# Optimization experiments

Measured on AMD Instinct MI355X. Metric: run time of the kernel, lower is better.

## Reference

```python
import jax, jax.numpy as jnp
import numpy as np

T, B, Z, ADIM = 96, 128, 32, 16
LEVELS, FACTOR = 3, 2


def setup_inputs() -> dict:
    key = jax.random.key(0)
    k1, k2, k3, k4 = jax.random.split(key, 4)
    eye = jnp.eye(Z, dtype=jnp.float32)
    obs = jax.random.normal(k1, (T, B, ADIM), jnp.float32)
    # A, D initialized near identity (module inits self.A/self.D as eye per level)
    A = eye + 0.02 * jax.random.normal(k2, (B, T, LEVELS, Z, Z), jnp.float32)
    C = 0.05 * jax.random.normal(k3, (B, T, ADIM, Z), jnp.float32)
    D = eye + 0.02 * jax.random.normal(k4, (B, T, LEVELS - 1, Z, Z), jnp.float32)
    return {"obs": obs, "A": A, "C": C, "D": D}


def _forward(obs, A, C, D):
    Tn, Bn, a_dim = obs.shape
    z = A.shape[-1]
    I = jnp.eye(z, dtype=obs.dtype)
    Q = 0.08 * I                              # process noise (z x z)
    O = 0.08 * I                              # higher-level process noise
    R = 0.03 * jnp.eye(a_dim, dtype=obs.dtype)
    sigma0 = 20.0 * I
    mu0 = jnp.zeros((Bn, z, 1), dtype=obs.dtype)
    obs_c = obs[..., None]                    # [T,B,a,1]

    # ---- higher-level latent chains (levels=3 => level indices {0,1}) ----
    f2 = FACTOR ** (LEVELS - 1)               # factor_level for l = levels-2
    mu_j = mu0 + 0.01                         # [B,z,1]
    # level 1 (top coupling level): mean jumps every f2 steps via A[:,t,levels-1]
    A2 = jnp.moveaxis(A[:, :, LEVELS - 1], 1, 0)   # [T,B,z,z]
    nj = (Tn - 1) // f2
    jump_A = A2[f2 * jnp.arange(1, nj + 1)]        # [nj,B,z,z]

    def jstep(m, At):
        mn = At @ m
        return mn, mn

    _, ms = jax.lax.scan(jstep, mu_j, jump_A)
    chain = jnp.concatenate([mu_j[None], ms], axis=0)      # [nj+1,B,z,1]
    tidx = jnp.arange(Tn)
    mean1 = chain[tidx // f2]                              # [T,B,z,1]
    # variance of level 1: sigma0 until the first jump, then zeros (faithful to source)
    var1 = jnp.broadcast_to(
        jnp.where((tidx < f2)[:, None, None, None], sigma0[None, None], 0.0),
        (Tn, Bn, z, z)).astype(obs.dtype)
    # level 0: mean stays zero; variance gets O from t>=FACTOR onward (faithful)
    mean0 = jnp.zeros((Tn, Bn, z, 1), dtype=obs.dtype)
    var0 = jnp.broadcast_to(
        jnp.where((tidx >= FACTOR)[:, None, None, None], O[None, None], 0.0),
        (Tn, Bn, z, z)).astype(obs.dtype)
    latent_means = jnp.stack([mean0, mean1], axis=2)       # [T,B,levels-1,z,1]
    latent_variances = jnp.stack([var0, var1], axis=2)     # [T,B,levels-1,z,z]

    # ---- main Kalman filter recursion over T ----
    C_t = jnp.moveaxis(C, 1, 0)                            # [T,B,a,z]
    A0 = jnp.moveaxis(A[:, :, 0], 1, 0)                    # [T,B,z,z]
    D0 = jnp.moveaxis(D[:, :, 0], 1, 0)                    # [T,B,z,z]
    pad_I = jnp.broadcast_to(I, (1, Bn, z, z))
    A_next = jnp.concatenate([A0[1:], pad_I], axis=0)      # A[:,t+1,0]; last unused
    D_next = jnp.concatenate([D0[1:], jnp.zeros_like(pad_I)], axis=0)

    def step(carry, xs):
        mu_t, sigma_t = carry
        o, Ct, An, Dn, m1, v1 = xs
        CT = jnp.swapaxes(Ct, -1, -2)
        r = o - Ct @ mu_t                                  # innovation [B,a,1]
        S = Ct @ sigma_t @ CT + R                          # [B,a,a]
        K = sigma_t @ CT @ jnp.linalg.inv(S)               # Kalman gain [B,z,a]
        mu_z = mu_t + K @ r
        I_ = I - K @ Ct
        sigma_z = I_ @ sigma_t @ jnp.swapaxes(I_, -1, -2) + K @ R @ jnp.swapaxes(K, -1, -2)
        mu_n = An @ mu_z + Dn @ m1
        sigma_n = An @ sigma_z @ jnp.swapaxes(An, -1, -2) + Q + Dn @ v1 @ jnp.swapaxes(Dn, -1, -2)
        return (mu_n, sigma_n), (mu_t, sigma_t, mu_z, sigma_z, S)

    init = (mu0, jnp.broadcast_to(sigma0, (Bn, z, z)).astype(obs.dtype))
    _, (mu_pred, sigma_pred, mu_filt, sigma_filt, S_tensor) = jax.lax.scan(
        step, init, (obs_c, C_t, A_next, D_next, mean1, var1))
    return (mu_filt, sigma_filt, mu_pred, sigma_pred,
            latent_means, latent_variances, S_tensor)


def reference(obs, A, C, D):
    return _forward(obs, A, C, D)
```

## Files before the change

### kernel.cpp

```cpp
#include <hip/hip_runtime.h>

typedef unsigned int uint;
typedef unsigned short ushort;

#define TT 96
#define BB 128

#define OFF_MUF   0
#define OFF_SIGF  393216
#define OFF_MUP   12976128
#define OFF_SIGP  13369344
#define OFF_LM    25952256
#define OFF_LV    26738688
#define OFF_ST    51904512

__device__ __forceinline__ float bf2f(uint u) {
  union { uint i; float f; } c; c.i = u << 16; return c.f;
}
__device__ __forceinline__ float bflo(uint w) { return bf2f(w & 0xffffu); }
__device__ __forceinline__ float bfhi(uint w) { return bf2f(w >> 16); }

__device__ __forceinline__ ushort f2bf(float f) {
  union { float f; uint i; } c; c.f = f;
  return (ushort)((c.i + 0x7fffu + ((c.i >> 16) & 1u)) >> 16);
}
__device__ __forceinline__ uint pack2(float a, float b) {
  return (uint)f2bf(a) | ((uint)f2bf(b) << 16);
}

__device__ __forceinline__ void split3(float x, ushort& h, ushort& m, ushort& l) {
  h = f2bf(x); float r = x - bf2f((uint)h);
  m = f2bf(r); r -= bf2f((uint)m);
  l = f2bf(r);
}

__device__ __forceinline__ float readlane_f(float x, int l) {
  return __int_as_float(__builtin_amdgcn_readlane(__float_as_int(x), l));
}

template<int F32>
__device__ __forceinline__ float4 ld4(const void* p, long e) {
  if constexpr (F32) {
    return *(const float4*)((const float*)p + e);
  } else {
    uint2 w = *(const uint2*)((const ushort*)p + e);
    return make_float4(bflo(w.x), bfhi(w.x), bflo(w.y), bfhi(w.y));
  }
}
template<int F32>
__device__ __forceinline__ float ld1(const void* p, long e) {
  if constexpr (F32) return ((const float*)p)[e];
  else               return bf2f((uint)((const ushort*)p)[e]);
}
template<int F32>
__device__ __forceinline__ void st4(void* p, long e, float4 v) {
  if constexpr (F32) {
    *(float4*)((float*)p + e) = v;
  } else {
    uint2 w; w.x = pack2(v.x, v.y); w.y = pack2(v.z, v.w);
    *(uint2*)((ushort*)p + e) = w;
  }
}
template<int F32>
__device__ __forceinline__ void st1(void* p, long e, float v) {
  if constexpr (F32) ((float*)p)[e] = v;
  else               ((ushort*)p)[e] = f2bf(v);
}

__device__ __forceinline__ bool data_is_f32(const void* A) {
  ushort h = ((const ushort*)A)[1];
  return (h & 0x7FFF) >= 0x3E80;
}

#define BAR() do { \
  __builtin_amdgcn_sched_barrier(0); \
  asm volatile("s_waitcnt lgkmcnt(0)" ::: "memory"); \
  __builtin_amdgcn_s_barrier(); \
  asm volatile("" ::: "memory"); \
  __builtin_amdgcn_sched_barrier(0); \
} while (0)

template<int F32>
__global__ void __launch_bounds__(256)
hkv_kernel(const void* __restrict__ obs, const void* __restrict__ A,
           const void* __restrict__ C, const void* __restrict__ D,
           void* __restrict__ out)
{
  if (data_is_f32(A) != (F32 == 1)) return;
  const int tid = threadIdx.x;

  if (blockIdx.x >= BB) {
    const int fb = blockIdx.x - BB;
    const int NG = (TT * BB * 2 * 32 * 32) / 4;
    for (int g = fb * 256 + tid; g < NG; g += BB * 256) {
      int e0 = g << 2;
      int R  = e0 >> 5;
      int c0 = e0 & 31;
      int zi = R & 31;
      int l  = (R >> 5) & 1;
      int t  = R >> 13;
      float dv = 0.0f;
      if (l == 0) { if (t >= 2) dv = 0.08f; }
      else        { if (t < 4)  dv = 20.0f; }
      float4 w = make_float4(0.f, 0.f, 0.f, 0.f);
      if (dv != 0.0f && zi >= c0 && zi < c0 + 4) ((float*)&w)[zi - c0] = dv;
      st4<F32>(out, OFF_LV + (long)e0, w);
    }
    return;
  }

  const int b    = blockIdx.x;
  const int lane = tid & 63;
  const int wv   = tid >> 6;

  __shared__ __align__(16) float sig[32][36];
  __shared__ __align__(16) float an[32][36];
  __shared__ __align__(16) float ant[32][36];
  __shared__ __align__(16) float dnm[32][36];
  __shared__ __align__(16) float asig[32][36];
  __shared__ __align__(16) float asAt[32][36];
  __shared__ __align__(16) float ct[16][36];
  __shared__ __align__(16) float cts[16][36];
  __shared__ __align__(16) float Vm[16][36];
  __shared__ __align__(16) float Ks[32][20];
  __shared__ __align__(16) float Um[32][20];
  __shared__ __align__(16) float Ss[16][20];
  __shared__ __align__(16) float ch[24][32];
  __shared__ float muv[32], muz[32], rv[16], yv[16], ov[16];

  for (int idx = tid; idx < 1024; idx += 256) {
    int i = idx >> 5, j = idx & 31;
    sig[i][j] = (i == j) ? 20.0f : 0.0f;
  }
  if (tid < 32) muv[tid] = 0.0f;

  if (tid < 32) {
    const int zi = tid;
    float m = 0.01f;
    ch[0][zi] = m;
    float cur[32], nxt[32];
    {
      long base = (((long)b * TT + 4) * 3 + 2) * 1024 + zi * 32;
      #pragma unroll
      for (int u = 0; u < 8; ++u) {
        float4 v = ld4<F32>(A, base + u * 4);
        nxt[4*u] = v.x; nxt[4*u+1] = v.y; nxt[4*u+2] = v.z; nxt[4*u+3] = v.w;
      }
    }
    for (int j = 1; j < 24; ++j) {
      #pragma unroll
      for (int u = 0; u < 32; ++u) cur[u] = nxt[u];
      if (j < 23) {
        long base = (((long)b * TT + 4 * (j + 1)) * 3 + 2) * 1024 + zi * 32;
        #pragma unroll
        for (int u = 0; u < 8; ++u) {
          float4 v = ld4<F32>(A, base + u * 4);
          nxt[4*u] = v.x; nxt[4*u+1] = v.y; nxt[4*u+2] = v.z; nxt[4*u+3] = v.w;
        }
      }
      float mp = m;
      float s = 0.0f;
      #pragma unroll
      for (int k = 0; k < 32; ++k) s = fmaf(cur[k], __shfl(mp, k, 64), s);
      m = s;
      ch[j][zi] = m;
    }
  }
  __syncthreads();

  for (int t = 0; t < TT; ++t) {
    const long tb = (long)t * BB + b;

    {
      int e0 = tid << 2;
      int i = e0 >> 5, j0 = e0 & 31;
      st4<F32>(out, OFF_SIGP + tb * 1024 + e0,
               make_float4(sig[i][j0], sig[i][j0+1], sig[i][j0+2], sig[i][j0+3]));
    }
    if (t < TT - 1) {
      int e0 = tid << 2; int i = e0 >> 5, j = e0 & 31;
      float4 a4 = ld4<F32>(A, ((long)(b * TT + t + 1) * 3) * 1024 + e0);
      an[i][j] = a4.x; an[i][j+1] = a4.y; an[i][j+2] = a4.z; an[i][j+3] = a4.w;
      ant[j][i] = a4.x; ant[j+1][i] = a4.y; ant[j+2][i] = a4.z; ant[j+3][i] = a4.w;
      float4 d4 = ld4<F32>(D, ((long)(b * TT + t + 1) * 2) * 1024 + e0);
      dnm[i][j] = d4.x; dnm[i][j+1] = d4.y; dnm[i][j+2] = d4.z; dnm[i][j+3] = d4.w;
    } else {
      int e0 = tid << 2; int i = e0 >> 5, j = e0 & 31;
      #pragma unroll
      for (int u = 0; u < 4; ++u) {
        float v = (i == j + u) ? 1.0f : 0.0f;
        an[i][j + u] = v; ant[j + u][i] = v; dnm[i][j + u] = 0.0f;
      }
    }
    if (tid < 128) {
      int e0 = tid << 2; int i = e0 >> 5, j = e0 & 31;
      float4 c4 = ld4<F32>(C, ((long)b * TT + t) * 512 + e0);
      ct[i][j] = c4.x; ct[i][j+1] = c4.y; ct[i][j+2] = c4.z; ct[i][j+3] = c4.w;
    } else if (tid < 192) {
      int l = (tid - 128) >> 5, zi = tid & 31;
      st1<F32>(out, OFF_LM + (tb * 2 + l) * 32 + zi, l ? ch[t >> 2][zi] : 0.0f);
    } else if (tid < 224) {
      int i = tid - 192;
      st1<F32>(out, OFF_MUP + tb * 32 + i, muv[i]);
    } else if (tid < 240) {
      int i = tid - 224;
      ov[i] = ld1<F32>(obs, tb * 16 + i);
    }
    __syncthreads();

    if (tid < 128) {
      int i = tid >> 3, j0 = (tid & 7) << 2;
      float4 acc = make_float4(0.f, 0.f, 0.f, 0.f);
      for (int k = 0; k < 32; ++k) {
        float a = ct[i][k];
        float4 s4 = *(const float4*)&sig[k][j0];
        acc.x = fmaf(a, s4.x, acc.x); acc.y = fmaf(a, s4.y, acc.y);
        acc.z = fmaf(a, s4.z, acc.z); acc.w = fmaf(a, s4.w, acc.w);
      }
      *(float4*)&cts[i][j0] = acc;
    } else if (tid < 144) {
      int i = tid - 128;
      float s = ov[i];
      for (int k = 0; k < 32; ++k) s = fmaf(-ct[i][k], muv[k], s);
      rv[i] = s;
    }
    __syncthreads();

    {
      int i = tid >> 4, j = tid & 15;
      float s = (i == j) ? 0.03f : 0.0f;
      for (int k = 0; k < 32; k += 4) {
        float4 a4 = *(const float4*)&cts[i][k];
        float4 b4 = *(const float4*)&ct[j][k];
        s += a4.x * b4.x + a4.y * b4.y + a4.z * b4.z + a4.w * b4.w;
      }
      Ss[i][j] = s;
      st1<F32>(out, OFF_ST + tb * 256 + tid, s);
    }
    __syncthreads();

    if (wv == 0) {
      const int r = lane >> 2, q = lane & 3;
      float v[13];
      #pragma unroll
      for (int m = 0; m < 13; ++m) {
        int c = 4 * m + q;
        float x = 0.0f;
        if (c < 16) x = Ss[r][c];
        else if (c < 48) x = cts[r][c - 16];
        else if (c == 48) x = rv[r];
        v[m] = x;
      }
      #pragma unroll
      for (int p = 0; p < 16; ++p) {
        const int mp = p >> 2, qp = p & 3;
        float pv = __shfl(v[mp], 4 * p + qp, 64);
        float f  = __shfl(v[mp], 4 * r + qp, 64);
        float rc = 1.0f / pv;
        #pragma unroll
        for (int m = 0; m < 13; ++m) {
          float srow = __shfl(v[m], 4 * p + q, 64) * rc;
          v[m] = (r == p) ? srow : fmaf(-f, srow, v[m]);
        }
      }
      #pragma unroll
      for (int m = 0; m < 13; ++m) {
        int c = 4 * m + q;
        if (c >= 16 && c < 48) Ks[c - 16][r] = v[m];
        else if (c == 48) yv[r] = v[m];
      }
    } else {
      int tt = tid - 64;
      for (int idx = tt; idx < 256; idx += 192) {
        int i = idx >> 3, j0 = (idx & 7) << 2;
        float4 acc = make_float4(0.f, 0.f, 0.f, 0.f);
        for (int k = 0; k < 32; ++k) {
          float a = an[i][k];
          float4 s4 = *(const float4*)&sig[k][j0];
          acc.x = fmaf(a, s4.x, acc.x); acc.y = fmaf(a, s4.y, acc.y);
          acc.z = fmaf(a, s4.z, acc.z); acc.w = fmaf(a, s4.w, acc.w);
        }
        *(float4*)&asig[i][j0] = acc;
      }
      for (int idx = tt; idx < 512; idx += 192) {
        int i = idx >> 5, j = idx & 31;
        float s = 0.0f;
        for (int k = 0; k < 32; k += 4) {
          float4 c4 = *(const float4*)&cts[i][k];
          float4 a4 = *(const float4*)&an[j][k];
          s += c4.x * a4.x + c4.y * a4.y + c4.z * a4.z + c4.w * a4.w;
        }
        Vm[i][j] = s;
      }
    }
    __syncthreads();

    {
      int i = tid >> 3, j0 = (tid & 7) << 2;
      float4 acc = make_float4(0.f, 0.f, 0.f, 0.f);
      for (int k = 0; k < 32; ++k) {
        float a = asig[i][k];
        float4 s4 = *(const float4*)&ant[k][j0];
        acc.x = fmaf(a, s4.x, acc.x); acc.y = fmaf(a, s4.y, acc.y);
        acc.z = fmaf(a, s4.z, acc.z); acc.w = fmaf(a, s4.w, acc.w);
      }
      int dd = i - j0;
      if (dd == 0) acc.x += 0.08f; else if (dd == 1) acc.y += 0.08f;
      else if (dd == 2) acc.z += 0.08f; else if (dd == 3) acc.w += 0.08f;
      *(float4*)&asAt[i][j0] = acc;

      float4 sz = *(const float4*)&sig[i][j0];
      for (int k = 0; k < 16; ++k) {
        float a = Ks[i][k];
        float4 c4 = *(const float4*)&cts[k][j0];
        sz.x = fmaf(-a, c4.x, sz.x); sz.y = fmaf(-a, c4.y, sz.y);
        sz.z = fmaf(-a, c4.z, sz.z); sz.w = fmaf(-a, c4.w, sz.w);
      }
      st4<F32>(out, OFF_SIGF + tb * 1024 + (i * 32 + j0), sz);
    }
    if (tid < 128) {
      int i = tid >> 2, j0 = (tid & 3) << 2;
      float4 acc = make_float4(0.f, 0.f, 0.f, 0.f);
      for (int k = 0; k < 32; ++k) {
        float a = an[i][k];
        float4 k4 = *(const float4*)&Ks[k][j0];
        acc.x = fmaf(a, k4.x, acc.x); acc.y = fmaf(a, k4.y, acc.y);
        acc.z = fmaf(a, k4.z, acc.z); acc.w = fmaf(a, k4.w, acc.w);
      }
      *(float4*)&Um[i][j0] = acc;
    } else if (tid < 160) {
      int i = tid - 128;
      float s = muv[i];
      for (int k = 0; k < 16; ++k) s = fmaf(cts[k][i], yv[k], s);
      muz[i] = s;
      st1<F32>(out, OFF_MUF + tb * 32 + i, s);
    }
    __syncthreads();

    {
      int i = tid >> 3, j0 = (tid & 7) << 2;
      float4 acc = *(const float4*)&asAt[i][j0];
      for (int k = 0; k < 16; ++k) {
        float u = Um[i][k];
        float4 v4 = *(const float4*)&Vm[k][j0];
        acc.x = fmaf(-u, v4.x, acc.x); acc.y = fmaf(-u, v4.y, acc.y);
        acc.z = fmaf(-u, v4.z, acc.z); acc.w = fmaf(-u, v4.w, acc.w);
      }
      if (t < 4) {
        float4 da = make_float4(0.f, 0.f, 0.f, 0.f);
        for (int k = 0; k < 32; ++k) {
          float a = dnm[i][k];
          da.x = fmaf(a, dnm[j0][k],     da.x);
          da.y = fmaf(a, dnm[j0 + 1][k], da.y);
          da.z = fmaf(a, dnm[j0 + 2][k], da.z);
          da.w = fmaf(a, dnm[j0 + 3][k], da.w);
        }
        acc.x += 20.0f * da.x; acc.y += 20.0f * da.y;
        acc.z += 20.0f * da.z; acc.w += 20.0f * da.w;
      }
      *(float4*)&sig[i][j0] = acc;
    }
    if (tid < 32) {
      int i = tid;
      float s = 0.0f;
      for (int k = 0; k < 32; ++k) s = fmaf(an[i][k], muz[k], s);
      const float* chr = ch[t >> 2];
      for (int k = 0; k < 32; ++k) s = fmaf(dnm[i][k], chr[k], s);
      muv[i] = s;
    }
    __syncthreads();
  }
}

typedef __attribute__((ext_vector_type(8))) short bf16x8;
typedef __attribute__((ext_vector_type(4))) float f32x4;

#define MFMA16(a, b, c) __builtin_amdgcn_mfma_f32_16x16x32_bf16((a), (b), (c), 0, 0, 0)

__global__ void __launch_bounds__(256)
hkv_f32(const void* __restrict__ obs, const void* __restrict__ A,
        const void* __restrict__ C, const void* __restrict__ D,
        void* __restrict__ out)
{
  if (!data_is_f32(A)) return;
  const int tid = threadIdx.x;
  float* outf = (float*)out;

  if (blockIdx.x >= BB) {
    const int fb = blockIdx.x - BB;
    const int NG = (TT * BB * 2 * 32 * 32) / 4;
    for (int g = fb * 256 + tid; g < NG; g += BB * 256) {
      int e0 = g << 2;
      int R  = e0 >> 5;
      int c0 = e0 & 31;
      int zi = R & 31;
      int l  = (R >> 5) & 1;
      int t  = R >> 13;
      float dv = 0.0f;
      if (l == 0) { if (t >= 2) dv = 0.08f; }
      else        { if (t < 4)  dv = 20.0f; }
      float4 w = make_float4(0.f, 0.f, 0.f, 0.f);
      if (dv != 0.0f && zi >= c0 && zi < c0 + 4) ((float*)&w)[zi - c0] = dv;
      st4<1>(out, OFF_LV + (long)e0, w);
    }
    return;
  }

  const int b    = blockIdx.x;
  const int lane = tid & 63;
  const int wv   = tid >> 6;
  const int tm   = wv >> 1;
  const int tn   = wv & 1;
  const int lr   = lane & 15;
  const int lk   = lane >> 4;
  const int lk8  = lk << 3;
  const int pi   = tid >> 3;
  const int pj   = (tid & 7) << 2;

  const float* Of = (const float*)obs;

  __shared__ __align__(16) ushort sg[3][32][40];
  __shared__ __align__(16) ushort an[3][32][40];
  __shared__ __align__(16) ushort dn[3][32][40];
  __shared__ __align__(16) ushort as_[3][32][40];
  __shared__ __align__(16) ushort ct[3][16][40];
  __shared__ __align__(16) ushort wt[3][16][40];
  __shared__ __align__(16) ushort kt[3][16][40];
  __shared__ __align__(16) ushort w_[3][32][24];
  __shared__ __align__(16) ushort ks[3][32][24];
  __shared__ __align__(16) ushort u_[3][32][24];
  __shared__ __align__(16) ushort aw[3][32][24];
  __shared__ __align__(16) float Ssf[16][20];
  __shared__ __align__(16) float wtf[16][36];
  __shared__ __align__(16) float ch[24][32];
  __shared__ __align__(16) float muv[32];
  __shared__ __align__(16) float muzv[32];
  __shared__ __align__(16) float rv[16];
  __shared__ __align__(16) float yv[16];
  __shared__ __align__(16) float ov[16];

  const bf16x8 z8 = {0, 0, 0, 0, 0, 0, 0, 0};
  #define F40(arr, rb) (*(const bf16x8*)&(arr)[(rb) + lr][lk8])
  #define F24(arr, rb) ((lk < 2) ? (*(const bf16x8*)&(arr)[(rb) + lr][lk8]) : z8)
  #define PROD_F(acc, X, xb, Y, yb) do { \
    bf16x8 xh_=F40(X[0],(xb)), xm_=F40(X[1],(xb)), xl_=F40(X[2],(xb)); \
    bf16x8 yh_=F40(Y[0],(yb)), ym_=F40(Y[1],(yb)), yl_=F40(Y[2],(yb)); \
    f32x4 a1_ = {0.f,0.f,0.f,0.f}; \
    acc=MFMA16(xh_,yh_,acc); a1_=MFMA16(xm_,yh_,a1_); \
    acc=MFMA16(xh_,ym_,acc); a1_=MFMA16(xl_,yh_,a1_); \
    acc=MFMA16(xh_,yl_,acc); a1_=MFMA16(xm_,ym_,a1_); \
    acc += a1_; } while(0)
  #define PROD_H(acc, X, xb, Y, yb) do { \
    bf16x8 xh_=F24(X[0],(xb)), xm_=F24(X[1],(xb)), xl_=F24(X[2],(xb)); \
    bf16x8 yh_=F24(Y[0],(yb)), ym_=F24(Y[1],(yb)), yl_=F24(Y[2],(yb)); \
    f32x4 a1_ = {0.f,0.f,0.f,0.f}; \
    acc=MFMA16(xh_,yh_,acc); a1_=MFMA16(xm_,yh_,a1_); \
    acc=MFMA16(xh_,ym_,acc); a1_=MFMA16(xl_,yh_,a1_); \
    acc=MFMA16(xh_,yl_,acc); a1_=MFMA16(xm_,ym_,a1_); \
    acc += a1_; } while(0)
  #define SPLW(ARR, rr, cc, x) do { ushort h_,m_,l_; split3((x),h_,m_,l_); \
    ARR[0][rr][cc]=h_; ARR[1][rr][cc]=m_; ARR[2][rr][cc]=l_; } while(0)

  float anc[4], dnc[4];
  {
    float4 a4 = ld4<1>(A, ((long)(b * TT + 1) * 3) * 1024 + (tid << 2));
    float4 d4 = ld4<1>(D, ((long)(b * TT + 1) * 2) * 1024 + (tid << 2));
    anc[0]=a4.x; anc[1]=a4.y; anc[2]=a4.z; anc[3]=a4.w;
    dnc[0]=d4.x; dnc[1]=d4.y; dnc[2]=d4.z; dnc[3]=d4.w;
    #pragma unroll
    for (int u = 0; u < 4; ++u) { SPLW(an, pi, pj+u, anc[u]); SPLW(dn, pi, pj+u, dnc[u]); }
  }
  if (tid < 128) {
    float4 c4 = ld4<1>(C, ((long)b * TT) * 512 + (tid << 2));
    float cc4[4] = {c4.x, c4.y, c4.z, c4.w};
    #pragma unroll
    for (int u = 0; u < 4; ++u) SPLW(ct, tid >> 3, ((tid & 7) << 2) + u, cc4[u]);
  } else if (tid < 144) {
    ov[tid - 128] = Of[(long)b * 16 + (tid - 128)];
  }
  for (int idx = tid; idx < 1024; idx += 256) {
    int i = idx >> 5, j = idx & 31;
    sg[0][i][j] = (i == j) ? 0x41A0 : 0;
    sg[1][i][j] = 0; sg[2][i][j] = 0;
  }
  if (tid < 32) muv[tid] = 0.0f;

  float sig_reg[4];
  #pragma unroll
  for (int v = 0; v < 4; ++v) {
    int rr = 16 * tm + lk * 4 + v, cc = 16 * tn + lr;
    sig_reg[v] = (rr == cc) ? 20.0f : 0.0f;
  }

  if (tid < 32) {
    const int zi = tid;
    float m = 0.01f;
    ch[0][zi] = m;
    float curv[32], nxtv[32];
    {
      long base = (((long)b * TT + 4) * 3 + 2) * 1024 + zi * 32;
      #pragma unroll
      for (int u = 0; u < 8; ++u) {
        float4 v = ld4<1>(A, base + u * 4);
        nxtv[4*u]=v.x; nxtv[4*u+1]=v.y; nxtv[4*u+2]=v.z; nxtv[4*u+3]=v.w;
      }
    }
    for (int j = 1; j < 24; ++j) {
      #pragma unroll
      for (int u = 0; u < 32; ++u) curv[u] = nxtv[u];
      if (j < 23) {
        long base = (((long)b * TT + 4 * (j + 1)) * 3 + 2) * 1024 + zi * 32;
        #pragma unroll
        for (int u = 0; u < 8; ++u) {
          float4 v = ld4<1>(A, base + u * 4);
          nxtv[4*u]=v.x; nxtv[4*u+1]=v.y; nxtv[4*u+2]=v.z; nxtv[4*u+3]=v.w;
        }
      }
      float mp = m, s = 0.0f;
      #pragma unroll
      for (int k = 0; k < 32; ++k) s = fmaf(curv[k], __shfl(mp, k, 64), s);
      m = s;
      ch[j][zi] = m;
    }
  }
  BAR();

  for (int t = 0; t < TT; ++t) {
    const long tb = (long)t * BB + b;

    {
      f32x4 acc = {0.f, 0.f, 0.f, 0.f};
      PROD_F(acc, an, 16 * tm, sg, 16 * tn);
      #pragma unroll
      for (int v = 0; v < 4; ++v) {
        int rr = 16 * tm + lk * 4 + v, cc = 16 * tn + lr;
        outf[OFF_SIGP + tb * 1024 + rr * 32 + cc] = sig_reg[v];
        SPLW(as_, rr, cc, acc[v]);
      }
    }
    if (wv >= 2) {
      const int a = wv - 2;
      f32x4 acc = {0.f, 0.f, 0.f, 0.f};
      PROD_F(acc, sg, 16 * a, ct, 0);
      #pragma unroll
      for (int v = 0; v < 4; ++v) {
        int row = 16 * a + lk * 4 + v;
        ushort h_, m_, l_; split3(acc[v], h_, m_, l_);
        w_[0][row][lr]=h_; w_[1][row][lr]=m_; w_[2][row][lr]=l_;
        wt[0][lr][row]=h_; wt[1][lr][row]=m_; wt[2][lr][row]=l_;
        wtf[lr][row] = acc[v];
      }
    } else if (wv == 0) {
      int i = lane & 15, kg = lane >> 4;
      float s = 0.0f;
      #pragma unroll
      for (int u = 0; u < 8; ++u) {
        int k = kg * 8 + u;
        float cv = bf2f((uint)ct[0][i][k]) + bf2f((uint)ct[1][i][k])
                 + bf2f((uint)ct[2][i][k]);
        s = fmaf(cv, muv[k], s);
      }
      s += __shfl_xor(s, 16, 64);
      s += __shfl_xor(s, 32, 64);
      if (kg == 0) rv[i] = ov[i] - s;
    } else {
      int l = lane >> 5, zi = lane & 31;
      outf[OFF_LM + (tb * 2 + l) * 32 + zi] = l ? ch[t >> 2][zi] : 0.0f;
      if (lane < 32) outf[OFF_MUP + tb * 32 + zi] = muv[zi];
    }
    BAR();

    float pa[4], pd[4], pc[4] = {0.f,0.f,0.f,0.f}; float pobs = 0.f;
    if (t < TT - 1) {
      if (t < TT - 2) {
        float4 a4 = ld4<1>(A, ((long)(b * TT + t + 2) * 3) * 1024 + (tid << 2));
        float4 d4 = ld4<1>(D, ((long)(b * TT + t + 2) * 2) * 1024 + (tid << 2));
        pa[0]=a4.x; pa[1]=a4.y; pa[2]=a4.z; pa[3]=a4.w;
        pd[0]=d4.x; pd[1]=d4.y; pd[2]=d4.z; pd[3]=d4.w;
      } else {
        #pragma unroll
        for (int u = 0; u < 4; ++u) { pa[u] = (pi == pj + u) ? 1.0f : 0.0f; pd[u] = 0.0f; }
      }
      if (tid < 128) {
        float4 c4 = ld4<1>(C, ((long)b * TT + (t + 1)) * 512 + (tid << 2));
        pc[0]=c4.x; pc[1]=c4.y; pc[2]=c4.z; pc[3]=c4.w;
      } else if (tid < 144) {
        pobs = Of[((long)(t + 1) * BB + b) * 16 + (tid - 128)];
      }
    }

    f32x4 acc_at = {0.f, 0.f, 0.f, 0.f};
    PROD_F(acc_at, as_, 16 * tm, an, 16 * tn);
    f32x4 acc_d = {0.f, 0.f, 0.f, 0.f};
    if (t < 4) PROD_F(acc_d, dn, 16 * tm, dn, 16 * tn);

    if (wv == 0) {
      f32x4 s4 = {0.f, 0.f, 0.f, 0.f};
      PROD_F(s4, wt, 0, ct, 0);
      #pragma unroll
      for (int v = 0; v < 4; ++v) {
        int r = lk * 4 + v;
        float val = s4[v] + ((r == lr) ? 0.03f : 0.0f);
        Ssf[r][lr] = val;
        outf[OFF_ST + tb * 256 + r * 16 + lr] = val;
      }
      const int c = lane;
      float gv[16];
      if (c < 16) {
        #pragma unroll
        for (int r = 0; r < 16; ++r) gv[r] = Ssf[r][c];
      } else if (c < 48) {
        #pragma unroll
        for (int r = 0; r < 16; ++r) gv[r] = wtf[r][c - 16];
      } else if (c == 48) {
        #pragma unroll
        for (int r = 0; r < 16; ++r) gv[r] = rv[r];
      } else {
        #pragma unroll
        for (int r = 0; r < 16; ++r) gv[r] = 0.0f;
      }
      #pragma unroll
      for (int p = 0; p < 16; ++p) {
        float f[16];
        #pragma unroll
        for (int r = 0; r < 16; ++r) f[r] = readlane_f(gv[r], p);
        float rc = 1.0f / f[p];
        float srow = gv[p] * rc;
        #pragma unroll
        for (int r = 0; r < 16; ++r)
          if (r != p) gv[r] = fmaf(-f[r], srow, gv[r]);
        gv[p] = srow;
      }
      if (c >= 16 && c < 48) {
        const int z = c - 16;
        #pragma unroll
        for (int u = 0; u < 8; ++u) {
          ushort h0,m0,l0,h1,m1,l1;
          split3(gv[2*u],   h0, m0, l0);
          split3(gv[2*u+1], h1, m1, l1);
          ((uint*)&ks[0][z][0])[u] = (uint)h0 | ((uint)h1 << 16);
          ((uint*)&ks[1][z][0])[u] = (uint)m0 | ((uint)m1 << 16);
          ((uint*)&ks[2][z][0])[u] = (uint)l0 | ((uint)l1 << 16);
          kt[0][2*u][z] = h0; kt[0][2*u+1][z] = h1;
          kt[1][2*u][z] = m0; kt[1][2*u+1][z] = m1;
          kt[2][2*u][z] = l0; kt[2][2*u+1][z] = l1;
        }
      } else if (c == 48) {
        #pragma unroll
        for (int r = 0; r < 16; ++r) yv[r] = gv[r];
      }
    } else if (wv < 3) {
      const int a = wv - 1;
      f32x4 w4 = {0.f, 0.f, 0.f, 0.f};
      PROD_F(w4, an, 16 * a, wt, 0);
      #pragma unroll
      for (int v = 0; v < 4; ++v) SPLW(aw, 16 * a + lk * 4 + v, lr, w4[v]);
    }
    BAR();

    {
      f32x4 kw = {0.f, 0.f, 0.f, 0.f};
      PROD_H(kw, ks, 16 * tm, w_, 16 * tn);
      #pragma unroll
      for (int v = 0; v < 4; ++v) {
        int rr = 16 * tm + lk * 4 + v, cc = 16 * tn + lr;
        outf[OFF_SIGF + tb * 1024 + rr * 32 + cc] = sig_reg[v] - kw[v];
      }
    }
    if (wv >= 2) {
      const int a = wv - 2;
      f32x4 u4 = {0.f, 0.f, 0.f, 0.f};
      PROD_F(u4, an, 16 * a, kt, 0);
      #pragma unroll
      for (int v = 0; v < 4; ++v) SPLW(u_, 16 * a + lk * 4 + v, lr, u4[v]);
    } else if (wv == 1) {
      int i = lane & 31, kg = lane >> 5;
      float s = 0.0f;
      #pragma unroll
      for (int u = 0; u < 8; ++u) {
        int k = kg * 8 + u;
        float wk = bf2f((uint)w_[0][i][k]) + bf2f((uint)w_[1][i][k])
                 + bf2f((uint)w_[2][i][k]);
        s = fmaf(wk, yv[k], s);
      }
      s += __shfl_xor(s, 32, 64);
      if (kg == 0) {
        float m = muv[i] + s;
        muzv[i] = m;
        outf[OFF_MUF + tb * 32 + i] = m;
      }
    }
    BAR();

    {
      f32x4 uw = {0.f, 0.f, 0.f, 0.f};
      PROD_H(uw, u_, 16 * tm, aw, 16 * tn);
      #pragma unroll
      for (int v = 0; v < 4; ++v) {
        int rr = 16 * tm + lk * 4 + v, cc = 16 * tn + lr;
        float sp = acc_at[v] - uw[v];
        if (rr == cc) sp += 0.08f;
        if (t < 4) sp = fmaf(20.0f, acc_d[v], sp);
        sig_reg[v] = sp;
        SPLW(sg, rr, cc, sp);
      }
    }
    {
      const float* chr = ch[t >> 2];
      float part = 0.0f;
      #pragma unroll
      for (int u = 0; u < 4; ++u) {
        part = fmaf(anc[u], muzv[pj + u], part);
        part = fmaf(dnc[u], chr[pj + u], part);
      }
      part += __shfl_xor(part, 1, 64);
      part += __shfl_xor(part, 2, 64);
      part += __shfl_xor(part, 4, 64);
      if ((tid & 7) == 0) muv[pi] = part;
    }
    if (t < TT - 1) {
      #pragma unroll
      for (int u = 0; u < 4; ++u) {
        SPLW(an, pi, pj + u, pa[u]);
        SPLW(dn, pi, pj + u, pd[u]);
        anc[u] = pa[u]; dnc[u] = pd[u];
      }
      if (tid < 128) {
        #pragma unroll
        for (int u = 0; u < 4; ++u) SPLW(ct, tid >> 3, ((tid & 7) << 2) + u, pc[u]);
      } else if (tid < 144) {
        ov[tid - 128] = pobs;
      }
    }
    BAR();
  }
  #undef F40
  #undef F24
  #undef PROD_F
  #undef PROD_H
  #undef SPLW
}

extern "C" void kernel_launch(void* const* d_in, const int* in_sizes, int n_in,
                              void* d_out, int out_size, void* d_ws, size_t ws_size,
                              hipStream_t stream) {
  const void* obs = d_in[0];
  const void* A   = d_in[1];
  const void* C   = d_in[2];
  const void* D   = d_in[3];
  (void)in_sizes; (void)n_in; (void)out_size; (void)d_ws; (void)ws_size;

  hkv_kernel<0><<<dim3(2 * BB), dim3(256), 0, stream>>>(obs, A, C, D, d_out);
  hkv_f32<<<dim3(2 * BB), dim3(256), 0, stream>>>(obs, A, C, D, d_out);
}
```

Baseline: 819.3 us.

## Invert S only and form gain via MFMA; pack split-bf16 LDS writes

The Gauss-Jordan solve now inverts S against the identity (16 columns) instead of solving for all 32 W^T columns, and the Kalman gain and A·K products are formed afterwards with extra MFMA stages. This adds one barrier phase. The innovation and mean-update dot products move onto MFMA and register-held C values. Split-bf16 shared-memory writes are packed into 64-bit stores, and some matrices are stored transposed so they feed the MFMA operands directly. The aim is less serial solve work and fewer scattered LDS stores, at the cost of an extra synchronization step and more MFMA work per time step.

```diff
diff --git a/kernel.cpp b/kernel.cpp
--- a/kernel.cpp
+++ b/kernel.cpp
@@ -414,6 +414,7 @@
   const int lr   = lane & 15;
   const int lk   = lane >> 4;
   const int lk8  = lk << 3;
+  const int lk4  = lk << 2;
   const int pi   = tid >> 3;
   const int pj   = (tid & 7) << 2;
 
@@ -425,13 +426,12 @@
   __shared__ __align__(16) ushort as_[3][32][40];
   __shared__ __align__(16) ushort ct[3][16][40];
   __shared__ __align__(16) ushort wt[3][16][40];
-  __shared__ __align__(16) ushort kt[3][16][40];
+  __shared__ __align__(16) ushort sinv[3][16][40];
   __shared__ __align__(16) ushort w_[3][32][24];
+  __shared__ __align__(16) ushort aw[3][32][24];
   __shared__ __align__(16) ushort ks[3][32][24];
   __shared__ __align__(16) ushort u_[3][32][24];
-  __shared__ __align__(16) ushort aw[3][32][24];
   __shared__ __align__(16) float Ssf[16][20];
-  __shared__ __align__(16) float wtf[16][36];
   __shared__ __align__(16) float ch[24][32];
   __shared__ __align__(16) float muv[32];
   __shared__ __align__(16) float muzv[32];
@@ -440,41 +440,37 @@
   __shared__ __align__(16) float ov[16];
 
   const bf16x8 z8 = {0, 0, 0, 0, 0, 0, 0, 0};
-  #define F40(arr, rb) (*(const bf16x8*)&(arr)[(rb) + lr][lk8])
-  #define F24(arr, rb) ((lk < 2) ? (*(const bf16x8*)&(arr)[(rb) + lr][lk8]) : z8)
-  #define PROD_F(acc, X, xb, Y, yb) do { \
-    bf16x8 xh_=F40(X[0],(xb)), xm_=F40(X[1],(xb)), xl_=F40(X[2],(xb)); \
-    bf16x8 yh_=F40(Y[0],(yb)), ym_=F40(Y[1],(yb)), yl_=F40(Y[2],(yb)); \
+  #define FR40(P, rb) (*(const bf16x8*)&(P)[(rb) + lr][lk8])
+  #define FR24(P, rb) ((lk < 2) ? (*(const bf16x8*)&(P)[(rb) + lr][lk8]) : z8)
+  #define FRS(P)      ((lk < 2) ? (*(const bf16x8*)&(P)[lr][lk8]) : z8)
+  #define PROD6(acc, xh,xm,xl, yh,ym,yl) do { \
     f32x4 a1_ = {0.f,0.f,0.f,0.f}; \
-    acc=MFMA16(xh_,yh_,acc); a1_=MFMA16(xm_,yh_,a1_); \
-    acc=MFMA16(xh_,ym_,acc); a1_=MFMA16(xl_,yh_,a1_); \
-    acc=MFMA16(xh_,yl_,acc); a1_=MFMA16(xm_,ym_,a1_); \
+    acc=MFMA16(xh,yh,acc); a1_=MFMA16(xm,yh,a1_); \
+    acc=MFMA16(xh,ym,acc); a1_=MFMA16(xl,yh,a1_); \
+    acc=MFMA16(xh,yl,acc); a1_=MFMA16(xm,ym,a1_); \
     acc += a1_; } while(0)
-  #define PROD_H(acc, X, xb, Y, yb) do { \
-    bf16x8 xh_=F24(X[0],(xb)), xm_=F24(X[1],(xb)), xl_=F24(X[2],(xb)); \
-    bf16x8 yh_=F24(Y[0],(yb)), ym_=F24(Y[1],(yb)), yl_=F24(Y[2],(yb)); \
-    f32x4 a1_ = {0.f,0.f,0.f,0.f}; \
-    acc=MFMA16(xh_,yh_,acc); a1_=MFMA16(xm_,yh_,a1_); \
-    acc=MFMA16(xh_,ym_,acc); a1_=MFMA16(xl_,yh_,a1_); \
-    acc=MFMA16(xh_,yl_,acc); a1_=MFMA16(xm_,ym_,a1_); \
-    acc += a1_; } while(0)
-  #define SPLW(ARR, rr, cc, x) do { ushort h_,m_,l_; split3((x),h_,m_,l_); \
-    ARR[0][rr][cc]=h_; ARR[1][rr][cc]=m_; ARR[2][rr][cc]=l_; } while(0)
-
-  float anc[4], dnc[4];
+  #define PACKW(ARR, rr, c0, x0, x1, x2, x3) do { \
+    ushort h0_,m0_,l0_,h1_,m1_,l1_,h2_,m2_,l2_,h3_,m3_,l3_; \
+    split3((x0),h0_,m0_,l0_); split3((x1),h1_,m1_,l1_); \
+    split3((x2),h2_,m2_,l2_); split3((x3),h3_,m3_,l3_); \
+    *(uint2*)&ARR[0][rr][c0] = make_uint2((uint)h0_|((uint)h1_<<16),(uint)h2_|((uint)h3_<<16)); \
+    *(uint2*)&ARR[1][rr][c0] = make_uint2((uint)m0_|((uint)m1_<<16),(uint)m2_|((uint)m3_<<16)); \
+    *(uint2*)&ARR[2][rr][c0] = make_uint2((uint)l0_|((uint)l1_<<16),(uint)l2_|((uint)l3_<<16)); \
+  } while(0)
+
+  float anc[4], dnc[4], ccur[4] = {0.f,0.f,0.f,0.f};
   {
     float4 a4 = ld4<1>(A, ((long)(b * TT + 1) * 3) * 1024 + (tid << 2));
     float4 d4 = ld4<1>(D, ((long)(b * TT + 1) * 2) * 1024 + (tid << 2));
     anc[0]=a4.x; anc[1]=a4.y; anc[2]=a4.z; anc[3]=a4.w;
     dnc[0]=d4.x; dnc[1]=d4.y; dnc[2]=d4.z; dnc[3]=d4.w;
-    #pragma unroll
-    for (int u = 0; u < 4; ++u) { SPLW(an, pi, pj+u, anc[u]); SPLW(dn, pi, pj+u, dnc[u]); }
+    PACKW(an, pi, pj, anc[0], anc[1], anc[2], anc[3]);
+    PACKW(dn, pi, pj, dnc[0], dnc[1], dnc[2], dnc[3]);
   }
   if (tid < 128) {
     float4 c4 = ld4<1>(C, ((long)b * TT) * 512 + (tid << 2));
-    float cc4[4] = {c4.x, c4.y, c4.z, c4.w};
-    #pragma unroll
-    for (int u = 0; u < 4; ++u) SPLW(ct, tid >> 3, ((tid & 7) << 2) + u, cc4[u]);
+    ccur[0]=c4.x; ccur[1]=c4.y; ccur[2]=c4.z; ccur[3]=c4.w;
+    PACKW(ct, (tid >> 3), ((tid & 7) << 2), ccur[0], ccur[1], ccur[2], ccur[3]);
   } else if (tid < 144) {
     ov[tid - 128] = Of[(long)b * 16 + (tid - 128)];
   }
@@ -488,7 +484,7 @@
   float sig_reg[4];
   #pragma unroll
   for (int v = 0; v < 4; ++v) {
-    int rr = 16 * tm + lk * 4 + v, cc = 16 * tn + lr;
+    int rr = 16 * tm + lk4 + v, cc = 16 * tn + lr;
     sig_reg[v] = (rr == cc) ? 20.0f : 0.0f;
   }
 
@@ -529,44 +525,43 @@
     const long tb = (long)t * BB + b;
 
     {
-      f32x4 acc = {0.f, 0.f, 0.f, 0.f};
-      PROD_F(acc, an, 16 * tm, sg, 16 * tn);
-      #pragma unroll
-      for (int v = 0; v < 4; ++v) {
-        int rr = 16 * tm + lk * 4 + v, cc = 16 * tn + lr;
-        outf[OFF_SIGP + tb * 1024 + rr * 32 + cc] = sig_reg[v];
-        SPLW(as_, rr, cc, acc[v]);
-      }
-    }
-    if (wv >= 2) {
+      bf16x8 xh = FR40(sg[0], 16*tm), xm = FR40(sg[1], 16*tm), xl = FR40(sg[2], 16*tm);
+      bf16x8 yh = FR40(an[0], 16*tn), ym = FR40(an[1], 16*tn), yl = FR40(an[2], 16*tn);
+      f32x4 pq = {0.f,0.f,0.f,0.f};
+      PROD6(pq, xh,xm,xl, yh,ym,yl);
+      #pragma unroll
+      for (int v = 0; v < 4; ++v)
+        outf[OFF_SIGP + tb * 1024 + (16*tm + lk4 + v) * 32 + (16*tn + lr)] = sig_reg[v];
+      PACKW(as_, 16*tn + lr, 16*tm + lk4, pq[0], pq[1], pq[2], pq[3]);
+    }
+    if (wv < 2) {
+      const int J = wv;
+      bf16x8 xh = FR40(ct[0], 0), xm = FR40(ct[1], 0), xl = FR40(ct[2], 0);
+      bf16x8 yh = FR40(sg[0], 16*J), ym = FR40(sg[1], 16*J), yl = FR40(sg[2], 16*J);
+      f32x4 q = {0.f,0.f,0.f,0.f};
+      PROD6(q, xh,xm,xl, yh,ym,yl);
+      PACKW(w_, 16*J + lr, lk4, q[0], q[1], q[2], q[3]);
+      float4 m4 = *(const float4*)&muv[pj];
+      float part = ccur[0]*m4.x;
+      part = fmaf(ccur[1], m4.y, part);
+      part = fmaf(ccur[2], m4.z, part);
+      part = fmaf(ccur[3], m4.w, part);
+      part += __shfl_xor(part, 1, 64);
+      part += __shfl_xor(part, 2, 64);
+      part += __shfl_xor(part, 4, 64);
+      if ((tid & 7) == 0) rv[pi] = ov[pi] - part;
+    } else {
       const int a = wv - 2;
-      f32x4 acc = {0.f, 0.f, 0.f, 0.f};
-      PROD_F(acc, sg, 16 * a, ct, 0);
-      #pragma unroll
-      for (int v = 0; v < 4; ++v) {
-        int row = 16 * a + lk * 4 + v;
-        ushort h_, m_, l_; split3(acc[v], h_, m_, l_);
-        w_[0][row][lr]=h_; w_[1][row][lr]=m_; w_[2][row][lr]=l_;
-        wt[0][lr][row]=h_; wt[1][lr][row]=m_; wt[2][lr][row]=l_;
-        wtf[lr][row] = acc[v];
-      }
-    } else if (wv == 0) {
-      int i = lane & 15, kg = lane >> 4;
-      float s = 0.0f;
-      #pragma unroll
-      for (int u = 0; u < 8; ++u) {
-        int k = kg * 8 + u;
-        float cv = bf2f((uint)ct[0][i][k]) + bf2f((uint)ct[1][i][k])
-                 + bf2f((uint)ct[2][i][k]);
-        s = fmaf(cv, muv[k], s);
-      }
-      s += __shfl_xor(s, 16, 64);
-      s += __shfl_xor(s, 32, 64);
-      if (kg == 0) rv[i] = ov[i] - s;
-    } else {
-      int l = lane >> 5, zi = lane & 31;
-      outf[OFF_LM + (tb * 2 + l) * 32 + zi] = l ? ch[t >> 2][zi] : 0.0f;
-      if (lane < 32) outf[OFF_MUP + tb * 32 + zi] = muv[zi];
+      bf16x8 xh = FR40(sg[0], 16*a), xm = FR40(sg[1], 16*a), xl = FR40(sg[2], 16*a);
+      bf16x8 yh = FR40(ct[0], 0), ym = FR40(ct[1], 0), yl = FR40(ct[2], 0);
+      f32x4 q = {0.f,0.f,0.f,0.f};
+      PROD6(q, xh,xm,xl, yh,ym,yl);
+      PACKW(wt, lr, 16*a + lk4, q[0], q[1], q[2], q[3]);
+      if (wv == 3) {
+        int l = lane >> 5, zi = lane & 31;
+        outf[OFF_LM + (tb * 2 + l) * 32 + zi] = l ? ch[t >> 2][zi] : 0.0f;
+        if (lane < 32) outf[OFF_MUP + tb * 32 + zi] = muv[zi];
+      }
     }
     BAR();
 
@@ -589,17 +584,29 @@
       }
     }
 
-    f32x4 acc_at = {0.f, 0.f, 0.f, 0.f};
-    PROD_F(acc_at, as_, 16 * tm, an, 16 * tn);
-    f32x4 acc_d = {0.f, 0.f, 0.f, 0.f};
-    if (t < 4) PROD_F(acc_d, dn, 16 * tm, dn, 16 * tn);
+    f32x4 acc_at = {0.f,0.f,0.f,0.f};
+    {
+      bf16x8 xh = FR40(as_[0], 16*tm), xm = FR40(as_[1], 16*tm), xl = FR40(as_[2], 16*tm);
+      bf16x8 yh = FR40(an[0], 16*tn), ym = FR40(an[1], 16*tn), yl = FR40(an[2], 16*tn);
+      PROD6(acc_at, xh,xm,xl, yh,ym,yl);
+    }
+    f32x4 acc_d = {0.f,0.f,0.f,0.f};
+    if (t < 4) {
+      bf16x8 xh = FR40(dn[0], 16*tm), xm = FR40(dn[1], 16*tm), xl = FR40(dn[2], 16*tm);
+      bf16x8 yh = FR40(dn[0], 16*tn), ym = FR40(dn[1], 16*tn), yl = FR40(dn[2], 16*tn);
+      PROD6(acc_d, xh,xm,xl, yh,ym,yl);
+    }
 
     if (wv == 0) {
-      f32x4 s4 = {0.f, 0.f, 0.f, 0.f};
-      PROD_F(s4, wt, 0, ct, 0);
+      f32x4 s4 = {0.f,0.f,0.f,0.f};
+      {
+        bf16x8 xh = FR40(ct[0], 0), xm = FR40(ct[1], 0), xl = FR40(ct[2], 0);
+        bf16x8 yh = FR40(wt[0], 0), ym = FR40(wt[1], 0), yl = FR40(wt[2], 0);
+        PROD6(s4, xh,xm,xl, yh,ym,yl);
+      }
       #pragma unroll
       for (int v = 0; v < 4; ++v) {
-        int r = lk * 4 + v;
+        int r = lk4 + v;
         float val = s4[v] + ((r == lr) ? 0.03f : 0.0f);
         Ssf[r][lr] = val;
         outf[OFF_ST + tb * 256 + r * 16 + lr] = val;
@@ -609,10 +616,10 @@
       if (c < 16) {
         #pragma unroll
         for (int r = 0; r < 16; ++r) gv[r] = Ssf[r][c];
-      } else if (c < 48) {
-        #pragma unroll
-        for (int r = 0; r < 16; ++r) gv[r] = wtf[r][c - 16];
-      } else if (c == 48) {
+      } else if (c < 32) {
+        #pragma unroll
+        for (int r = 0; r < 16; ++r) gv[r] = (r == c - 16) ? 1.0f : 0.0f;
+      } else if (c == 32) {
         #pragma unroll
         for (int r = 0; r < 16; ++r) gv[r] = rv[r];
       } else {
@@ -631,114 +638,130 @@
           if (r != p) gv[r] = fmaf(-f[r], srow, gv[r]);
         gv[p] = srow;
       }
-      if (c >= 16 && c < 48) {
-        const int z = c - 16;
-        #pragma unroll
-        for (int u = 0; u < 8; ++u) {
-          ushort h0,m0,l0,h1,m1,l1;
-          split3(gv[2*u],   h0, m0, l0);
-          split3(gv[2*u+1], h1, m1, l1);
-          ((uint*)&ks[0][z][0])[u] = (uint)h0 | ((uint)h1 << 16);
-          ((uint*)&ks[1][z][0])[u] = (uint)m0 | ((uint)m1 << 16);
-          ((uint*)&ks[2][z][0])[u] = (uint)l0 | ((uint)l1 << 16);
-          kt[0][2*u][z] = h0; kt[0][2*u+1][z] = h1;
-          kt[1][2*u][z] = m0; kt[1][2*u+1][z] = m1;
-          kt[2][2*u][z] = l0; kt[2][2*u+1][z] = l1;
+      if (c >= 16 && c < 32) {
+        const int j = c - 16;
+        #pragma unroll
+        for (int u = 0; u < 4; ++u) {
+          ushort h0,m0,l0,h1,m1,l1,h2,m2,l2,h3,m3,l3;
+          split3(gv[4*u+0], h0,m0,l0); split3(gv[4*u+1], h1,m1,l1);
+          split3(gv[4*u+2], h2,m2,l2); split3(gv[4*u+3], h3,m3,l3);
+          *(uint2*)&sinv[0][j][4*u] = make_uint2((uint)h0|((uint)h1<<16),(uint)h2|((uint)h3<<16));
+          *(uint2*)&sinv[1][j][4*u] = make_uint2((uint)m0|((uint)m1<<16),(uint)m2|((uint)m3<<16));
+          *(uint2*)&sinv[2][j][4*u] = make_uint2((uint)l0|((uint)l1<<16),(uint)l2|((uint)l3<<16));
         }
-      } else if (c == 48) {
-        #pragma unroll
-        for (int r = 0; r < 16; ++r) yv[r] = gv[r];
-      }
+      }
+      float myy = 0.0f;
+      #pragma unroll
+      for (int r = 0; r < 16; ++r) {
+        float s = readlane_f(gv[r], 32);
+        if (lane == r) myy = s;
+      }
+      if (lane < 16) yv[lane] = myy;
     } else if (wv < 3) {
-      const int a = wv - 1;
-      f32x4 w4 = {0.f, 0.f, 0.f, 0.f};
-      PROD_F(w4, an, 16 * a, wt, 0);
-      #pragma unroll
-      for (int v = 0; v < 4; ++v) SPLW(aw, 16 * a + lk * 4 + v, lr, w4[v]);
+      const int J = wv - 1;
+      bf16x8 xh = FR40(wt[0], 0), xm = FR40(wt[1], 0), xl = FR40(wt[2], 0);
+      bf16x8 yh = FR40(an[0], 16*J), ym = FR40(an[1], 16*J), yl = FR40(an[2], 16*J);
+      f32x4 q = {0.f,0.f,0.f,0.f};
+      PROD6(q, xh,xm,xl, yh,ym,yl);
+      PACKW(aw, 16*J + lr, lk4, q[0], q[1], q[2], q[3]);
     }
     BAR();
 
-    {
-      f32x4 kw = {0.f, 0.f, 0.f, 0.f};
-      PROD_H(kw, ks, 16 * tm, w_, 16 * tn);
+    if (wv < 2) {
+      const int J = wv;
+      bf16x8 sh = FRS(sinv[0]), sm = FRS(sinv[1]), sl = FRS(sinv[2]);
+      bf16x8 wh = FR24(w_[0], 16*J), wm = FR24(w_[1], 16*J), wl = FR24(w_[2], 16*J);
+      f32x4 kq = {0.f,0.f,0.f,0.f};
+      PROD6(kq, sh,sm,sl, wh,wm,wl);
+      PACKW(ks, 16*J + lr, lk4, kq[0], kq[1], kq[2], kq[3]);
+      bf16x8 ayh = z8, aym = z8, ayl = z8;
+      if (lr == 0 && lk < 2) {
+        #pragma unroll
+        for (int e = 0; e < 8; ++e) {
+          ushort h_, m_, l_; split3(yv[lk8 + e], h_, m_, l_);
+          ayh[e] = (short)h_; aym[e] = (short)m_; ayl[e] = (short)l_;
+        }
+      }
+      f32x4 mq = {0.f,0.f,0.f,0.f};
+      PROD6(mq, ayh,aym,ayl, wh,wm,wl);
+      if (lk == 0) {
+        float m = muv[16*J + lr] + mq[0];
+        muzv[16*J + lr] = m;
+        outf[OFF_MUF + tb * 32 + 16*J + lr] = m;
+      }
+    } else {
+      const int J = wv - 2;
+      bf16x8 sh = FRS(sinv[0]), sm = FRS(sinv[1]), sl = FRS(sinv[2]);
+      bf16x8 bh = FR24(aw[0], 16*J), bm = FR24(aw[1], 16*J), bl = FR24(aw[2], 16*J);
+      f32x4 uq = {0.f,0.f,0.f,0.f};
+      PROD6(uq, sh,sm,sl, bh,bm,bl);
+      PACKW(u_, 16*J + lr, lk4, uq[0], uq[1], uq[2], uq[3]);
+    }
+    BAR();
+
+    {
+      bf16x8 xh = FR24(ks[0], 16*tm), xm = FR24(ks[1], 16*tm), xl = FR24(ks[2], 16*tm);
+      bf16x8 yh = FR24(w_[0], 16*tn), ym = FR24(w_[1], 16*tn), yl = FR24(w_[2], 16*tn);
+      f32x4 kw = {0.f,0.f,0.f,0.f};
+      PROD6(kw, xh,xm,xl, yh,ym,yl);
+      #pragma unroll
+      for (int v = 0; v < 4; ++v)
+        outf[OFF_SIGF + tb * 1024 + (16*tm + lk4 + v) * 32 + (16*tn + lr)] = sig_reg[v] - kw[v];
+    }
+    {
+      bf16x8 xh = FR24(u_[0], 16*tm), xm = FR24(u_[1], 16*tm), xl = FR24(u_[2], 16*tm);
+      bf16x8 yh = FR24(aw[0], 16*tn), ym = FR24(aw[1], 16*tn), yl = FR24(aw[2], 16*tn);
+      f32x4 uw = {0.f,0.f,0.f,0.f};
+      PROD6(uw, xh,xm,xl, yh,ym,yl);
+      float sp4[4];
       #pragma unroll
       for (int v = 0; v < 4; ++v) {
-        int rr = 16 * tm + lk * 4 + v, cc = 16 * tn + lr;
-        outf[OFF_SIGF + tb * 1024 + rr * 32 + cc] = sig_reg[v] - kw[v];
-      }
-    }
-    if (wv >= 2) {
-      const int a = wv - 2;
-      f32x4 u4 = {0.f, 0.f, 0.f, 0.f};
-      PROD_F(u4, an, 16 * a, kt, 0);
-      #pragma unroll
-      for (int v = 0; v < 4; ++v) SPLW(u_, 16 * a + lk * 4 + v, lr, u4[v]);
-    } else if (wv == 1) {
-      int i = lane & 31, kg = lane >> 5;
-      float s = 0.0f;
-      #pragma unroll
-      for (int u = 0; u < 8; ++u) {
-        int k = kg * 8 + u;
-        float wk = bf2f((uint)w_[0][i][k]) + bf2f((uint)w_[1][i][k])
-                 + bf2f((uint)w_[2][i][k]);
-        s = fmaf(wk, yv[k], s);
-      }
-      s += __shfl_xor(s, 32, 64);
-      if (kg == 0) {
-        float m = muv[i] + s;
-        muzv[i] = m;
-        outf[OFF_MUF + tb * 32 + i] = m;
-      }
-    }
-    BAR();
-
-    {
-      f32x4 uw = {0.f, 0.f, 0.f, 0.f};
-      PROD_H(uw, u_, 16 * tm, aw, 16 * tn);
-      #pragma unroll
-      for (int v = 0; v < 4; ++v) {
-        int rr = 16 * tm + lk * 4 + v, cc = 16 * tn + lr;
+        int rr = 16*tm + lk4 + v, cc = 16*tn + lr;
         float sp = acc_at[v] - uw[v];
         if (rr == cc) sp += 0.08f;
         if (t < 4) sp = fmaf(20.0f, acc_d[v], sp);
         sig_reg[v] = sp;
-        SPLW(sg, rr, cc, sp);
-      }
+        sp4[v] = sp;
+      }
+      PACKW(sg, 16*tn + lr, 16*tm + lk4, sp4[0], sp4[1], sp4[2], sp4[3]);
     }
     {
       const float* chr = ch[t >> 2];
-      float part = 0.0f;
-      #pragma unroll
-      for (int u = 0; u < 4; ++u) {
-        part = fmaf(anc[u], muzv[pj + u], part);
-        part = fmaf(dnc[u], chr[pj + u], part);
-      }
+      float4 mz4 = *(const float4*)&muzv[pj];
+      float4 ch4 = *(const float4*)&chr[pj];
+      float part = anc[0]*mz4.x;
+      part = fmaf(anc[1], mz4.y, part);
+      part = fmaf(anc[2], mz4.z, part);
+      part = fmaf(anc[3], mz4.w, part);
+      part = fmaf(dnc[0], ch4.x, part);
+      part = fmaf(dnc[1], ch4.y, part);
+      part = fmaf(dnc[2], ch4.z, part);
+      part = fmaf(dnc[3], ch4.w, part);
       part += __shfl_xor(part, 1, 64);
       part += __shfl_xor(part, 2, 64);
       part += __shfl_xor(part, 4, 64);
       if ((tid & 7) == 0) muv[pi] = part;
     }
     if (t < TT - 1) {
-      #pragma unroll
-      for (int u = 0; u < 4; ++u) {
-        SPLW(an, pi, pj + u, pa[u]);
-        SPLW(dn, pi, pj + u, pd[u]);
-        anc[u] = pa[u]; dnc[u] = pd[u];
-      }
+      PACKW(an, pi, pj, pa[0], pa[1], pa[2], pa[3]);
+      PACKW(dn, pi, pj, pd[0], pd[1], pd[2], pd[3]);
+      #pragma unroll
+      for (int u = 0; u < 4; ++u) { anc[u] = pa[u]; dnc[u] = pd[u]; }
       if (tid < 128) {
-        #pragma unroll
-        for (int u = 0; u < 4; ++u) SPLW(ct, tid >> 3, ((tid & 7) << 2) + u, pc[u]);
+        PACKW(ct, (tid >> 3), ((tid & 7) << 2), pc[0], pc[1], pc[2], pc[3]);
+        #pragma unroll
+        for (int u = 0; u < 4; ++u) ccur[u] = pc[u];
       } else if (tid < 144) {
         ov[tid - 128] = pobs;
       }
     }
     BAR();
   }
-  #undef F40
-  #undef F24
-  #undef PROD_F
-  #undef PROD_H
-  #undef SPLW
+  #undef FR40
+  #undef FR24
+  #undef FRS
+  #undef PROD6
+  #undef PACKW
 }
 
 extern "C" void kernel_launch(void* const* d_in, const int* in_sizes, int n_in,
```

Result: slower. 851.3 us (+3.9%).
